# Kernel optimization log

Hardware: AMD Instinct MI355X
Metric: run time of the kernel (lower is better)

## Reference

```python
import jax, jax.numpy as jnp
import numpy as np

B, T, D = 2, 2048, 1024
NH, NKV, HD = 16, 4, 64
BASE, TSL, QGI = 10000.0, 1024, 1.5
EPS = 1.1920929e-07  # torch.finfo(float32).eps used by F.rms_norm default


def _rope_cos_sin(seq_len, rd):
    # Rotary.forward with self.rd == head_dim (Attn sets rd=0 -> full rotation)
    if seq_len > TSL:  # NTK-style base rescale branch
        nb = BASE * (seq_len / TSL) ** (rd / (rd - 2))
    else:
        nb = BASE
    inv = 1.0 / nb ** (jnp.arange(0, rd, 2, dtype=jnp.float32) / rd)
    fr = jnp.arange(seq_len, dtype=jnp.float32)[:, None] * inv[None, :]
    return jnp.cos(fr)[None, :, None, :], jnp.sin(fr)[None, :, None, :]


def _apply_rope(x, cos, sin):
    h = x.shape[-1] // 2
    x1, x2 = x[..., :h], x[..., h:]
    return jnp.concatenate([x1 * cos + x2 * sin, -x1 * sin + x2 * cos], axis=-1)


def _rms_norm(x):
    return x * jax.lax.rsqrt(jnp.mean(x * x, axis=-1, keepdims=True) + EPS)


def setup_inputs() -> dict:
    key = jax.random.key(0)
    ks = jax.random.split(key, 8)
    s = jnp.float32(0.02)
    return {
        "x": jax.random.normal(ks[0], (B, T, D), jnp.float32),
        "qw": jax.random.normal(ks[1], (NH * HD, D), jnp.float32) * s,
        "kw": jax.random.normal(ks[2], (NKV * HD, D), jnp.float32) * s,
        "vw": jax.random.normal(ks[3], (NKV * HD, D), jnp.float32) * s,
        "ow": jax.random.normal(ks[4], (D, D), jnp.float32) * s,
        "ve": jax.random.normal(ks[5], (B, T, NKV * HD), jnp.float32) * s,
        "v0": jax.random.normal(ks[6], (B, T, NKV, HD), jnp.float32) * s,
        "q_gain": jnp.full((NH,), QGI, jnp.float32),
        "vr_lambda": jnp.array([0.5, 0.5], jnp.float32),
        "gate_w": jnp.zeros((NH, D), jnp.float32),      # nn.init.zeros_
        "gate_b": jnp.full((NH,), 4.0, jnp.float32),    # nn.init.constant_(4.0)
    }


def reference(x, qw, kw, vw, ow, ve, v0, q_gain, vr_lambda, gate_w, gate_b):
    # projections
    q = (x @ qw.T).reshape(B, T, NH, HD)
    k = (x @ kw.T).reshape(B, T, NKV, HD)
    v = (x @ vw.T + ve).reshape(B, T, NKV, HD)
    raw_v = v  # returned when vr=True
    v = vr_lambda[0] * v0 + vr_lambda[1] * v  # value residual
    # qk rms-norm + rope (full head dim since self.rd == 0) + per-head q gain
    q = _rms_norm(q)
    k = _rms_norm(k)
    cos, sin = _rope_cos_sin(T, HD)
    q = _apply_rope(q, cos, sin)
    k = _apply_rope(k, cos, sin)
    q = q * q_gain[None, None, :, None]
    # causal GQA attention (nh query heads share nkv kv heads)
    G = NH // NKV
    qg = q.reshape(B, T, NKV, G, HD)
    scale = 1.0 / np.sqrt(HD).astype(np.float32)
    scores = jnp.einsum('bqhgd,bkhd->bhgqk', qg, k) * scale  # [B,NKV,G,T,T]
    causal = jnp.tril(jnp.ones((T, T), bool))
    scores = jnp.where(causal[None, None, None], scores, jnp.finfo(scores.dtype).min)
    p = jax.nn.softmax(scores, axis=-1)
    y = jnp.einsum('bhgqk,bkhd->bqhgd', p, v).reshape(B, T, NH, HD)
    # gated attention output
    gate = jax.nn.sigmoid(x @ gate_w.T + gate_b)  # [B,T,NH]
    y = y * gate[..., None]
    out = y.reshape(B, T, D) @ ow.T
    return out, raw_v
```

## Files before the change

### kernel.cpp

```cpp
#include <hip/hip_runtime.h>
#include <math.h>

#define BB 2
#define TT 2048
#define DD 1024
#define NH 16
#define NKV 4
#define HD 64
#define EPSF 1.1920929e-07f
#define LOG2_NB 14.319970444065578
#define SCALE_LOG2E 0.18033688011112042f
#define FIXMAX 17.5f

typedef __attribute__((ext_vector_type(8))) short bf16x8;
typedef __attribute__((ext_vector_type(4))) float f32x4;

__device__ inline short f2bf(float f) {
    unsigned u = __builtin_bit_cast(unsigned, f);
    unsigned r = (u + 0x7fffu + ((u >> 16) & 1u)) >> 16;
    return (short)r;
}
__device__ inline float bf2f(short s) {
    unsigned u = ((unsigned)(unsigned short)s) << 16;
    return __builtin_bit_cast(float, u);
}
__device__ inline unsigned cvt_pk_bf16(float a, float b) {
    unsigned r;
    asm("v_cvt_pk_bf16_f32 %0, %1, %2" : "=v"(r) : "v"(a), "v"(b));
    return r;
}

__global__ __launch_bounds__(256) void conv_all(
    const float* __restrict__ x, const float* __restrict__ qw,
    const float* __restrict__ kw, const float* __restrict__ vw,
    const float* __restrict__ ow, const float* __restrict__ gw,
    short* __restrict__ x16, short* __restrict__ wb16, short* __restrict__ ow16)
{
    int i = blockIdx.x * 256 + threadIdx.x;
    if (i >= 1708032) {
        ((short4*)(wb16 + 1552*1024))[i - 1708032] = (short4){0,0,0,0};
        return;
    }
    const float* src; short* dst; int j;
    if (i < 1048576)      { src = x;  dst = x16;            j = i; }
    else if (i < 1310720) { src = qw; dst = wb16;           j = i - 1048576; }
    else if (i < 1376256) { src = kw; dst = wb16 + 1048576; j = i - 1310720; }
    else if (i < 1441792) { src = vw; dst = wb16 + 1310720; j = i - 1376256; }
    else if (i < 1703936) { src = ow; dst = ow16;           j = i - 1441792; }
    else                  { src = gw; dst = wb16 + 1572864; j = i - 1703936; }
    float4 v = ((const float4*)src)[j];
    short4 o;
    o.x = f2bf(v.x); o.y = f2bf(v.y); o.z = f2bf(v.z); o.w = f2bf(v.w);
    ((short4*)dst)[j] = o;
}

#define GSTAGE(buf, k0, Abase, Bbase)                                                   \
{                                                                                       \
    _Pragma("unroll")                                                                   \
    for (int i_ = 0; i_ < 2; i_++) {                                                    \
        int off = w*2048 + i_*1024;                      \
        int g = (off >> 4) + lane;                                   \
        int row = g >> 2, c = g & 3;                                                    \
        int cg = c ^ (row & 3);                                        \
        const short* ga = (Abase) + (size_t)(m0 + row)*1024 + (k0) + cg*8;              \
        __builtin_amdgcn_global_load_lds(                                               \
            (const __attribute__((address_space(1))) void*)ga,                          \
            (__attribute__((address_space(3))) void*)((char*)&As[buf][0] + off), 16, 0, 0); \
        const short* gb = (Bbase) + (size_t)(n0 + row)*1024 + (k0) + cg*8;              \
        __builtin_amdgcn_global_load_lds(                                               \
            (const __attribute__((address_space(1))) void*)gb,                          \
            (__attribute__((address_space(3))) void*)((char*)&Bs[buf][0] + off), 16, 0, 0); \
    }                                                                                   \
}

#define GEMM_MAIN_LOOP(kbeg, kend, Abase, Bbase)                                        \
    GSTAGE(0, (kbeg), (Abase), (Bbase));                                                \
    __syncthreads();                                                                    \
    for (int k0 = (kbeg); k0 < (kend); k0 += 32) {                                      \
        int cur = ((k0 - (kbeg)) >> 5) & 1;                                             \
        bf16x8 af[4], bfr[4];                                                           \
        _Pragma("unroll")                                                               \
        for (int tm = 0; tm < 4; tm++) {                                                \
            int row = wy*64 + tm*16 + lc;                                               \
            af[tm] = *(const bf16x8*)(&As[cur][0] + row*32 + ((quad*8) ^ ((row&3)*8))); \
        }                                                                               \
        _Pragma("unroll")                                                               \
        for (int tn = 0; tn < 4; tn++) {                                                \
            int row = wx*64 + tn*16 + lc;                                               \
            bfr[tn] = *(const bf16x8*)(&Bs[cur][0] + row*32 + ((quad*8) ^ ((row&3)*8))); \
        }                                                                               \
        if (k0 + 32 < (kend)) GSTAGE(cur ^ 1, k0 + 32, (Abase), (Bbase));               \
        _Pragma("unroll")                                                               \
        for (int tm = 0; tm < 4; tm++)                                                  \
            _Pragma("unroll")                                                           \
            for (int tn = 0; tn < 4; tn++)                                              \
                acc[tm][tn] = __builtin_amdgcn_mfma_f32_16x16x32_bf16(af[tm], bfr[tn], acc[tm][tn], 0, 0, 0); \
        __syncthreads();                                                                \
    }

__global__ __launch_bounds__(256, 3) void gemm_qkv_fused(
    const short* __restrict__ A, const short* __restrict__ Bmat,
    const float* __restrict__ ve, const float* __restrict__ v0,
    const float* __restrict__ q_gain, const float* __restrict__ vr_lambda,
    const float* __restrict__ gb_, float* __restrict__ gate,
    short* __restrict__ qbh, short* __restrict__ kbh, short* __restrict__ vtb,
    float* __restrict__ rawv)
{
    __shared__ short As[2][128*32];
    __shared__ short Bs[2][128*32];
    int tid = threadIdx.x;
    int w = tid >> 6, lane = tid & 63;
    int quad = lane >> 4, lc = lane & 15;
    int wy = w >> 1, wx = w & 1;
    int m0 = blockIdx.y * 128, n0 = blockIdx.x * 128;

    f32x4 acc[4][4];
    #pragma unroll
    for (int i = 0; i < 4; i++)
        #pragma unroll
        for (int j = 0; j < 4; j++) acc[i][j] = (f32x4){0.f,0.f,0.f,0.f};

    GEMM_MAIN_LOOP(0, 1024, A, Bmat);

    int hc = n0 + wx*64;
    if (hc < 1280) {
        bool isq = (hc < 1024);
        int h = isq ? (hc >> 6) : ((hc - 1024) >> 6);
        float gsc = isq ? (q_gain[h] * SCALE_LOG2E) : 1.0f;
        short* dst = isq ? qbh : kbh;
        int nhh = isq ? 16 : 4;
        float inv0 = (float)exp2((double)lc * (-LOG2_NB / 32.0));
        float inv1 = (float)exp2((double)(lc + 16) * (-LOG2_NB / 32.0));
        #pragma unroll
        for (int tm = 0; tm < 4; tm++) {
            #pragma unroll
            for (int r = 0; r < 4; r++) {
                int m = m0 + wy*64 + tm*16 + quad*4 + r;
                int b = m >> 11, t = m & (TT - 1);
                float a0 = acc[tm][0][r], a1 = acc[tm][1][r];
                float a2 = acc[tm][2][r], a3 = acc[tm][3][r];
                float ss = a0*a0 + a1*a1 + a2*a2 + a3*a3;
                ss += __shfl_xor(ss, 1);
                ss += __shfl_xor(ss, 2);
                ss += __shfl_xor(ss, 4);
                ss += __shfl_xor(ss, 8);
                float rn = rsqrtf(ss * (1.0f/64.0f) + EPSF);
                a0 *= rn; a1 *= rn; a2 *= rn; a3 *= rn;
                float sn0, cs0, sn1, cs1;
                sincosf((float)t * inv0, &sn0, &cs0);
                sincosf((float)t * inv1, &sn1, &cs1);
                float o0 = a0*cs0 + a2*sn0;
                float o1 = a1*cs1 + a3*sn1;
                float o2 = a2*cs0 - a0*sn0;
                float o3 = a3*cs1 - a1*sn1;
                size_t base = (((size_t)(b*nhh + h))*2048 + t)*64 + lc;
                dst[base +  0] = f2bf(o0 * gsc);
                dst[base + 16] = f2bf(o1 * gsc);
                dst[base + 32] = f2bf(o2 * gsc);
                dst[base + 48] = f2bf(o3 * gsc);
            }
        }
    } else if (hc < 1536) {
        int kvh = (hc - 1280) >> 6;
        float l0 = vr_lambda[0], l1 = vr_lambda[1];
        short* lbase = (w < 2) ? &As[w][0] : &Bs[w - 2][0];
        #pragma unroll
        for (int tm = 0; tm < 4; tm++) {
            #pragma unroll
            for (int r = 0; r < 4; r++) {
                int m = m0 + wy*64 + tm*16 + quad*4 + r;
                int tl = tm*16 + quad*4 + r;
                size_t off = (size_t)m*256 + kvh*64 + lc;
                #pragma unroll
                for (int tn = 0; tn < 4; tn++) {
                    int d = tn*16 + lc;
                    float val = acc[tm][tn][r] + ve[off + tn*16];
                    rawv[off + tn*16] = val;
                    lbase[d*64 + (tl ^ ((d & 7) * 8))] = f2bf(l0 * v0[off + tn*16] + l1 * val);
                }
            }
        }
        int b = m0 >> 11;
        int t0g = (m0 & 2047) + wy*64;
        short* vdst = vtb + (size_t)(b*4 + kvh)*64*2048;
        #pragma unroll
        for (int j = 0; j < 16; j++) {
            int d = quad + j*4;
            int tc = lc*4;
            short4 vv = *(const short4*)&lbase[d*64 + (tc ^ ((d & 7) * 8))];
            *(short4*)&vdst[(size_t)d*2048 + t0g + tc] = vv;
        }
    } else if (hc == 1536) {
        #pragma unroll
        for (int tm = 0; tm < 4; tm++)
            #pragma unroll
            for (int r = 0; r < 4; r++) {
                int m = m0 + wy*64 + tm*16 + quad*4 + r;
                float lg = acc[tm][0][r] + gb_[lc];
                gate[(size_t)m*16 + lc] = 1.0f / (1.0f + __expf(-lg));
            }
    }
}

__global__ __launch_bounds__(256, 4) void gemm_mfma(
    const short* __restrict__ A, const short* __restrict__ Bmat,
    float* __restrict__ C, int ldc, int klen)
{
    __shared__ short As[2][128*32];
    __shared__ short Bs[2][128*32];
    int tid = threadIdx.x;
    int w = tid >> 6, lane = tid & 63;
    int quad = lane >> 4, lc = lane & 15;
    int wy = w >> 1, wx = w & 1;
    int m0 = blockIdx.y * 128, n0 = blockIdx.x * 128;

    f32x4 acc[4][4];
    #pragma unroll
    for (int i = 0; i < 4; i++)
        #pragma unroll
        for (int j = 0; j < 4; j++) acc[i][j] = (f32x4){0.f,0.f,0.f,0.f};

    GEMM_MAIN_LOOP(0, klen, A, Bmat);

    #pragma unroll
    for (int tm = 0; tm < 4; tm++)
        #pragma unroll
        for (int r = 0; r < 4; r++) {
            int m = m0 + wy*64 + tm*16 + quad*4 + r;
            #pragma unroll
            for (int tn = 0; tn < 4; tn++) {
                int n = n0 + wx*64 + tn*16 + lc;
                C[(size_t)m*ldc + n] = acc[tm][tn][r];
            }
        }
}

__global__ __launch_bounds__(256, 4) void flash_mfma(
    const short* __restrict__ qbh, const short* __restrict__ kbh,
    const short* __restrict__ vtb, const float* __restrict__ gate,
    short* __restrict__ y16)
{
    __shared__ short Ks[2][64*64];
    __shared__ short Vt[2][64*64];
    __shared__ short Ps[4][16*64];

    int bh = blockIdx.x;
    int b = bh >> 4, h = bh & 15, kvh = h >> 2;
    int qt = 31 - blockIdx.y;
    int tid = threadIdx.x;
    int w = tid >> 6, lane = tid & 63;
    int quad = lane >> 4, lc = lane & 15;

    const short* qbase = qbh + (((size_t)bh)*2048 + qt*64 + w*16 + lc)*64;
    bf16x8 qf0 = *(const bf16x8*)(qbase + quad*8);
    bf16x8 qf1 = *(const bf16x8*)(qbase + 32 + quad*8);

    f32x4 o[4];
    #pragma unroll
    for (int i = 0; i < 4; i++) o[i] = (f32x4){0.f,0.f,0.f,0.f};
    f32x4 l4 = (f32x4){0.f,0.f,0.f,0.f};
    const bf16x8 ones = {(short)0x3F80,(short)0x3F80,(short)0x3F80,(short)0x3F80,
                         (short)0x3F80,(short)0x3F80,(short)0x3F80,(short)0x3F80};

    const size_t kbase = ((size_t)(b*4 + kvh))*2048*64;
    const size_t vbase = ((size_t)(b*4 + kvh))*64*2048;

    #define STAGE(buf, kt)                                                              \
    {                                                                                   \
        _Pragma("unroll")                                                               \
        for (int i = 0; i < 2; i++) {                                                   \
            int off = w*2048 + i*1024;                                                  \
            int g = (off >> 4) + lane;                                                  \
            int row = g >> 3, c = g & 7;                                                \
            int cg = c ^ (row & 7);                                                     \
            const short* gk = kbh + kbase + (size_t)((kt)*64 + row)*64 + cg*8;          \
            __builtin_amdgcn_global_load_lds(                                           \
                (const __attribute__((address_space(1))) void*)gk,                      \
                (__attribute__((address_space(3))) void*)((char*)Ks[buf] + off), 16, 0, 0); \
            const short* gv = vtb + vbase + (size_t)row*2048 + (kt)*64 + cg*8;          \
            __builtin_amdgcn_global_load_lds(                                           \
                (const __attribute__((address_space(1))) void*)gv,                      \
                (__attribute__((address_space(3))) void*)((char*)Vt[buf] + off), 16, 0, 0); \
        }                                                                               \
    }

    STAGE(0, 0);
    __syncthreads();

    short* ps = Ps[w];

    for (int kt = 0; kt <= qt; kt++) {
        int cur = kt & 1;
        bool diag = (kt == qt);

        bf16x8 kf0[4], kf1[4], vf0[4], vf1[4];
        #pragma unroll
        for (int kn = 0; kn < 4; kn++) {
            int row = kn*16 + lc;
            int sw = (row & 7) * 8;
            const short* kr = Ks[cur] + row*64;
            kf0[kn] = *(const bf16x8*)(kr + ((quad*8) ^ sw));
            kf1[kn] = *(const bf16x8*)(kr + ((quad*8 + 32) ^ sw));
            const short* vr = Vt[cur] + row*64;
            vf0[kn] = *(const bf16x8*)(vr + ((quad*8) ^ sw));
            vf1[kn] = *(const bf16x8*)(vr + ((quad*8 + 32) ^ sw));
        }
        if (kt < qt) STAGE(cur ^ 1, kt + 1);

        f32x4 s4[4];
        #pragma unroll
        for (int kn = 0; kn < 4; kn++) {
            f32x4 acc = (f32x4){0.f,0.f,0.f,0.f};
            acc = __builtin_amdgcn_mfma_f32_16x16x32_bf16(kf0[kn], qf0, acc, 0, 0, 0);
            acc = __builtin_amdgcn_mfma_f32_16x16x32_bf16(kf1[kn], qf1, acc, 0, 0, 0);
            s4[kn] = acc;
        }

        #pragma unroll
        for (int kn = 0; kn < 4; kn++) {
            float p0 = __builtin_amdgcn_exp2f(s4[kn][0] - FIXMAX);
            float p1 = __builtin_amdgcn_exp2f(s4[kn][1] - FIXMAX);
            float p2 = __builtin_amdgcn_exp2f(s4[kn][2] - FIXMAX);
            float p3 = __builtin_amdgcn_exp2f(s4[kn][3] - FIXMAX);
            if (diag) {
                int keyb = kn*16 + quad*4, qv = w*16 + lc;
                if (keyb + 0 > qv) p0 = 0.f;
                if (keyb + 1 > qv) p1 = 0.f;
                if (keyb + 2 > qv) p2 = 0.f;
                if (keyb + 3 > qv) p3 = 0.f;
            }
            int c = kn*4 + quad;
            int cs = c ^ ((lc & 7) << 1);
            int2 pk;
            pk.x = (int)cvt_pk_bf16(p0, p1);
            pk.y = (int)cvt_pk_bf16(p2, p3);
            *(int2*)(ps + lc*64 + cs*4) = pk;
        }
        __asm__ volatile("s_waitcnt lgkmcnt(0)" ::: "memory");
        int u0 = (0*4 + quad) ^ (lc & 7);
        int u1 = (1*4 + quad) ^ (lc & 7);
        bf16x8 pf0 = *(const bf16x8*)(ps + lc*64 + u0*8);
        bf16x8 pf1 = *(const bf16x8*)(ps + lc*64 + u1*8);

        #pragma unroll
        for (int dn = 0; dn < 4; dn++) {
            o[dn] = __builtin_amdgcn_mfma_f32_16x16x32_bf16(pf0, vf0[dn], o[dn], 0, 0, 0);
            o[dn] = __builtin_amdgcn_mfma_f32_16x16x32_bf16(pf1, vf1[dn], o[dn], 0, 0, 0);
        }
        l4 = __builtin_amdgcn_mfma_f32_16x16x32_bf16(pf0, ones, l4, 0, 0, 0);
        l4 = __builtin_amdgcn_mfma_f32_16x16x32_bf16(pf1, ones, l4, 0, 0, 0);
        __syncthreads();
    }

    #pragma unroll
    for (int r = 0; r < 4; r++) {
        int row = b*2048 + qt*64 + w*16 + quad*4 + r;
        float g = gate[(size_t)row*16 + h] / l4[r];
        #pragma unroll
        for (int dn = 0; dn < 4; dn++)
            y16[(size_t)row*1024 + h*64 + dn*16 + lc] = f2bf(o[dn][r] * g);
    }
}

extern "C" void kernel_launch(void* const* d_in, const int* in_sizes, int n_in,
                              void* d_out, int out_size, void* d_ws, size_t ws_size,
                              hipStream_t stream) {
    (void)in_sizes; (void)n_in; (void)out_size; (void)ws_size;
    const float* x  = (const float*)d_in[0];
    const float* qw = (const float*)d_in[1];
    const float* kw = (const float*)d_in[2];
    const float* vw = (const float*)d_in[3];
    const float* ow = (const float*)d_in[4];
    const float* ve = (const float*)d_in[5];
    const float* v0 = (const float*)d_in[6];
    const float* qg = (const float*)d_in[7];
    const float* vl = (const float*)d_in[8];
    const float* gw = (const float*)d_in[9];
    const float* gb = (const float*)d_in[10];

    float* out  = (float*)d_out;
    float* rawv = out + (size_t)BB*TT*DD;

    float* p    = (float*)d_ws;
    short* x16  = (short*)p;        p += 2097152;
    short* wb16 = (short*)p;        p += 851968;
    short* ow16 = (short*)p;        p += 524288;
    short* qbh  = (short*)p;        p += 2097152;
    short* kbh  = (short*)p;        p += 524288;
    short* vtb  = (short*)p;        p += 524288;
    float* gt   = p;                p += 65536;
    short* y16  = (short*)p;

    conv_all<<<6784, 256, 0, stream>>>(x, qw, kw, vw, ow, gw, x16, wb16, ow16);
    gemm_qkv_fused<<<dim3(13, 32), 256, 0, stream>>>(x16, wb16, ve, v0, qg, vl,
                                                     gb, gt, qbh, kbh, vtb, rawv);
    flash_mfma<<<dim3(32, 32), 256, 0, stream>>>(qbh, kbh, vtb, gt, y16);
    gemm_mfma<<<dim3(8, 32), 256, 0, stream>>>(y16, ow16, out, 1024, 1024);
}
```

Baseline: 186.1 us.

## Use 64x128 GEMM tiles with a three-stage LDS ring and vmcnt waits

```diff
diff --git a/kernel.cpp b/kernel.cpp
--- a/kernel.cpp
+++ b/kernel.cpp
@@ -19,10 +19,6 @@
     unsigned u = __builtin_bit_cast(unsigned, f);
     unsigned r = (u + 0x7fffu + ((u >> 16) & 1u)) >> 16;
     return (short)r;
-}
-__device__ inline float bf2f(short s) {
-    unsigned u = ((unsigned)(unsigned short)s) << 16;
-    return __builtin_bit_cast(float, u);
 }
 __device__ inline unsigned cvt_pk_bf16(float a, float b) {
     unsigned r;
@@ -54,51 +50,64 @@
     ((short4*)dst)[j] = o;
 }
 
-#define GSTAGE(buf, k0, Abase, Bbase)                                                   \
+#define GSTAGE64(Ab, Bb, k0, Abase, Bbase)                                              \
 {                                                                                       \
-    _Pragma("unroll")                                                                   \
-    for (int i_ = 0; i_ < 2; i_++) {                                                    \
-        int off = w*2048 + i_*1024;                      \
-        int g = (off >> 4) + lane;                                   \
+    {                                                                                   \
+        int g = w*64 + lane;                          \
         int row = g >> 2, c = g & 3;                                                    \
         int cg = c ^ (row & 3);                                        \
         const short* ga = (Abase) + (size_t)(m0 + row)*1024 + (k0) + cg*8;              \
         __builtin_amdgcn_global_load_lds(                                               \
             (const __attribute__((address_space(1))) void*)ga,                          \
-            (__attribute__((address_space(3))) void*)((char*)&As[buf][0] + off), 16, 0, 0); \
+            (__attribute__((address_space(3))) void*)((char*)(Ab) + w*1024), 16, 0, 0); \
+    }                                                                                   \
+    _Pragma("unroll")                                                                   \
+    for (int i_ = 0; i_ < 2; i_++) {                                                    \
+        int off = w*2048 + i_*1024;                                                     \
+        int g = (off >> 4) + lane;                                   \
+        int row = g >> 2, c = g & 3;                                                    \
+        int cg = c ^ (row & 3);                                                         \
         const short* gb = (Bbase) + (size_t)(n0 + row)*1024 + (k0) + cg*8;              \
         __builtin_amdgcn_global_load_lds(                                               \
             (const __attribute__((address_space(1))) void*)gb,                          \
-            (__attribute__((address_space(3))) void*)((char*)&Bs[buf][0] + off), 16, 0, 0); \
+            (__attribute__((address_space(3))) void*)((char*)(Bb) + off), 16, 0, 0);    \
     }                                                                                   \
 }
 
-#define GEMM_MAIN_LOOP(kbeg, kend, Abase, Bbase)                                        \
-    GSTAGE(0, (kbeg), (Abase), (Bbase));                                                \
-    __syncthreads();                                                                    \
-    for (int k0 = (kbeg); k0 < (kend); k0 += 32) {                                      \
-        int cur = ((k0 - (kbeg)) >> 5) & 1;                                             \
-        bf16x8 af[4], bfr[4];                                                           \
-        _Pragma("unroll")                                                               \
-        for (int tm = 0; tm < 4; tm++) {                                                \
-            int row = wy*64 + tm*16 + lc;                                               \
-            af[tm] = *(const bf16x8*)(&As[cur][0] + row*32 + ((quad*8) ^ ((row&3)*8))); \
+#define GEMM_RING64(KLEN, Abase, Bbase)                                                 \
+    GSTAGE64(&As[0][0], &Bs[0][0], 0,  (Abase), (Bbase));                               \
+    GSTAGE64(&As[1][0], &Bs[1][0], 32, (Abase), (Bbase));                               \
+    {                                                                                   \
+        int steps = (KLEN) >> 5;                                                        \
+        for (int st = 0; st < steps; st++) {                                            \
+            int k0 = st << 5;                                                           \
+            int cur = st % 3;                                                           \
+            if (st < steps - 1) asm volatile("s_waitcnt vmcnt(3)\n\ts_barrier" ::: "memory"); \
+            else                asm volatile("s_waitcnt vmcnt(0)\n\ts_barrier" ::: "memory"); \
+            bf16x8 af[2], bfr[4];                                                       \
+            _Pragma("unroll")                                                           \
+            for (int tm = 0; tm < 2; tm++) {                                            \
+                int row = wy*32 + tm*16 + lc;                                           \
+                af[tm] = *(const bf16x8*)(&As[cur][0] + row*32 + ((quad*8) ^ ((row&3)*8))); \
+            }                                                                           \
+            _Pragma("unroll")                                                           \
+            for (int tn = 0; tn < 4; tn++) {                                            \
+                int row = wx*64 + tn*16 + lc;                                           \
+                bfr[tn] = *(const bf16x8*)(&Bs[cur][0] + row*32 + ((quad*8) ^ ((row&3)*8))); \
+            }                                                                           \
+            if (st + 2 < steps) {                                                       \
+                int nxt = (st + 2) % 3;                                                 \
+                GSTAGE64(&As[nxt][0], &Bs[nxt][0], k0 + 64, (Abase), (Bbase));          \
+            }                                                                           \
+            _Pragma("unroll")                                                           \
+            for (int tm = 0; tm < 2; tm++)                                              \
+                _Pragma("unroll")                                                       \
+                for (int tn = 0; tn < 4; tn++)                                          \
+                    acc[tm][tn] = __builtin_amdgcn_mfma_f32_16x16x32_bf16(af[tm], bfr[tn], acc[tm][tn], 0, 0, 0); \
         }                                                                               \
-        _Pragma("unroll")                                                               \
-        for (int tn = 0; tn < 4; tn++) {                                                \
-            int row = wx*64 + tn*16 + lc;                                               \
-            bfr[tn] = *(const bf16x8*)(&Bs[cur][0] + row*32 + ((quad*8) ^ ((row&3)*8))); \
-        }                                                                               \
-        if (k0 + 32 < (kend)) GSTAGE(cur ^ 1, k0 + 32, (Abase), (Bbase));               \
-        _Pragma("unroll")                                                               \
-        for (int tm = 0; tm < 4; tm++)                                                  \
-            _Pragma("unroll")                                                           \
-            for (int tn = 0; tn < 4; tn++)                                              \
-                acc[tm][tn] = __builtin_amdgcn_mfma_f32_16x16x32_bf16(af[tm], bfr[tn], acc[tm][tn], 0, 0, 0); \
-        __syncthreads();                                                                \
-    }
-
-__global__ __launch_bounds__(256, 3) void gemm_qkv_fused(
+    }
+
+__global__ __launch_bounds__(256, 4) void gemm_qkv_fused(
     const short* __restrict__ A, const short* __restrict__ Bmat,
     const float* __restrict__ ve, const float* __restrict__ v0,
     const float* __restrict__ q_gain, const float* __restrict__ vr_lambda,
@@ -106,21 +115,22 @@
     short* __restrict__ qbh, short* __restrict__ kbh, short* __restrict__ vtb,
     float* __restrict__ rawv)
 {
-    __shared__ short As[2][128*32];
-    __shared__ short Bs[2][128*32];
+    __shared__ short As[3][64*32];
+    __shared__ short Bs[3][128*32];
     int tid = threadIdx.x;
     int w = tid >> 6, lane = tid & 63;
     int quad = lane >> 4, lc = lane & 15;
     int wy = w >> 1, wx = w & 1;
-    int m0 = blockIdx.y * 128, n0 = blockIdx.x * 128;
-
-    f32x4 acc[4][4];
+    int m0 = blockIdx.x * 64, n0 = blockIdx.y * 128;
+
+    f32x4 acc[2][4];
     #pragma unroll
-    for (int i = 0; i < 4; i++)
+    for (int i = 0; i < 2; i++)
         #pragma unroll
         for (int j = 0; j < 4; j++) acc[i][j] = (f32x4){0.f,0.f,0.f,0.f};
 
-    GEMM_MAIN_LOOP(0, 1024, A, Bmat);
+    GEMM_RING64(1024, A, Bmat);
+    __syncthreads();
 
     int hc = n0 + wx*64;
     if (hc < 1280) {
@@ -132,10 +142,10 @@
         float inv0 = (float)exp2((double)lc * (-LOG2_NB / 32.0));
         float inv1 = (float)exp2((double)(lc + 16) * (-LOG2_NB / 32.0));
         #pragma unroll
-        for (int tm = 0; tm < 4; tm++) {
+        for (int tm = 0; tm < 2; tm++) {
             #pragma unroll
             for (int r = 0; r < 4; r++) {
-                int m = m0 + wy*64 + tm*16 + quad*4 + r;
+                int m = m0 + wy*32 + tm*16 + quad*4 + r;
                 int b = m >> 11, t = m & (TT - 1);
                 float a0 = acc[tm][0][r], a1 = acc[tm][1][r];
                 float a2 = acc[tm][2][r], a3 = acc[tm][3][r];
@@ -163,12 +173,13 @@
     } else if (hc < 1536) {
         int kvh = (hc - 1280) >> 6;
         float l0 = vr_lambda[0], l1 = vr_lambda[1];
-        short* lbase = (w < 2) ? &As[w][0] : &Bs[w - 2][0];
-        #pragma unroll
-        for (int tm = 0; tm < 4; tm++) {
+        short* lbase = (w < 3) ? (short*)((char*)&As[0][0] + w*4096)
+                               : (short*)&Bs[0][0];
+        #pragma unroll
+        for (int tm = 0; tm < 2; tm++) {
             #pragma unroll
             for (int r = 0; r < 4; r++) {
-                int m = m0 + wy*64 + tm*16 + quad*4 + r;
+                int m = m0 + wy*32 + tm*16 + quad*4 + r;
                 int tl = tm*16 + quad*4 + r;
                 size_t off = (size_t)m*256 + kvh*64 + lc;
                 #pragma unroll
@@ -176,26 +187,26 @@
                     int d = tn*16 + lc;
                     float val = acc[tm][tn][r] + ve[off + tn*16];
                     rawv[off + tn*16] = val;
-                    lbase[d*64 + (tl ^ ((d & 7) * 8))] = f2bf(l0 * v0[off + tn*16] + l1 * val);
+                    lbase[d*32 + (tl ^ ((d & 7) * 4))] = f2bf(l0 * v0[off + tn*16] + l1 * val);
                 }
             }
         }
         int b = m0 >> 11;
-        int t0g = (m0 & 2047) + wy*64;
+        int t0g = (m0 & 2047) + wy*32;
         short* vdst = vtb + (size_t)(b*4 + kvh)*64*2048;
         #pragma unroll
         for (int j = 0; j < 16; j++) {
             int d = quad + j*4;
-            int tc = lc*4;
-            short4 vv = *(const short4*)&lbase[d*64 + (tc ^ ((d & 7) * 8))];
-            *(short4*)&vdst[(size_t)d*2048 + t0g + tc] = vv;
+            int tc = lc*2;
+            short2 vv = *(const short2*)&lbase[d*32 + (tc ^ ((d & 7) * 4))];
+            *(short2*)&vdst[(size_t)d*2048 + t0g + tc] = vv;
         }
     } else if (hc == 1536) {
         #pragma unroll
-        for (int tm = 0; tm < 4; tm++)
+        for (int tm = 0; tm < 2; tm++)
             #pragma unroll
             for (int r = 0; r < 4; r++) {
-                int m = m0 + wy*64 + tm*16 + quad*4 + r;
+                int m = m0 + wy*32 + tm*16 + quad*4 + r;
                 float lg = acc[tm][0][r] + gb_[lc];
                 gate[(size_t)m*16 + lc] = 1.0f / (1.0f + __expf(-lg));
             }
@@ -206,27 +217,27 @@
     const short* __restrict__ A, const short* __restrict__ Bmat,
     float* __restrict__ C, int ldc, int klen)
 {
-    __shared__ short As[2][128*32];
-    __shared__ short Bs[2][128*32];
+    __shared__ short As[3][64*32];
+    __shared__ short Bs[3][128*32];
     int tid = threadIdx.x;
     int w = tid >> 6, lane = tid & 63;
     int quad = lane >> 4, lc = lane & 15;
     int wy = w >> 1, wx = w & 1;
-    int m0 = blockIdx.y * 128, n0 = blockIdx.x * 128;
-
-    f32x4 acc[4][4];
+    int m0 = blockIdx.x * 64, n0 = blockIdx.y * 128;
+
+    f32x4 acc[2][4];
     #pragma unroll
-    for (int i = 0; i < 4; i++)
+    for (int i = 0; i < 2; i++)
         #pragma unroll
         for (int j = 0; j < 4; j++) acc[i][j] = (f32x4){0.f,0.f,0.f,0.f};
 
-    GEMM_MAIN_LOOP(0, klen, A, Bmat);
+    GEMM_RING64(klen, A, Bmat);
 
     #pragma unroll
-    for (int tm = 0; tm < 4; tm++)
+    for (int tm = 0; tm < 2; tm++)
         #pragma unroll
         for (int r = 0; r < 4; r++) {
-            int m = m0 + wy*64 + tm*16 + quad*4 + r;
+            int m = m0 + wy*32 + tm*16 + quad*4 + r;
             #pragma unroll
             for (int tn = 0; tn < 4; tn++) {
                 int n = n0 + wx*64 + tn*16 + lc;
@@ -360,6 +371,7 @@
         for (int dn = 0; dn < 4; dn++)
             y16[(size_t)row*1024 + h*64 + dn*16 + lc] = f2bf(o[dn][r] * g);
     }
+    #undef STAGE
 }
 
 extern "C" void kernel_launch(void* const* d_in, const int* in_sizes, int n_in,
@@ -392,8 +404,8 @@
     short* y16  = (short*)p;
 
     conv_all<<<6784, 256, 0, stream>>>(x, qw, kw, vw, ow, gw, x16, wb16, ow16);
-    gemm_qkv_fused<<<dim3(13, 32), 256, 0, stream>>>(x16, wb16, ve, v0, qg, vl,
+    gemm_qkv_fused<<<dim3(64, 13), 256, 0, stream>>>(x16, wb16, ve, v0, qg, vl,
                                                      gb, gt, qbh, kbh, vtb, rawv);
     flash_mfma<<<dim3(32, 32), 256, 0, stream>>>(qbh, kbh, vtb, gt, y16);
-    gemm_mfma<<<dim3(8, 32), 256, 0, stream>>>(y16, ow16, out, 1024, 1024);
-}
+    gemm_mfma<<<dim3(64, 8), 256, 0, stream>>>(y16, ow16, out, 1024, 1024);
+}
```

Measured after the change: 175.6 us. 5.7% less time.
